# Kernel optimization log

Measured on AMD Instinct MI355X. Metric: run time of the kernel, lower is better.

## Reference

```python
import jax, jax.numpy as jnp
from jax import lax
import numpy as np

N = 4096      # nnodes
D = 64        # embed_dim
R = 128       # nodes per region
G = N // R    # 32 regions (contiguous blocks)
BIG = 1e9     # 'no edge' cost (scipy MST treats zero-similarity entries as absent edges)


def setup_inputs() -> dict:
    key = jax.random.key(0)
    emb = jax.random.normal(key, (N, D), dtype=jnp.float32) * 0.05  # nn.Embedding weight (xavier-like scale)
    region_id = jnp.arange(N) // R
    inter_mask = (region_id[:, None] != region_id[None, :]).astype(jnp.float32)  # block off-diagonal buffer
    return {"emb_weight": emb, "inter_mask": inter_mask, "inter_budget": 1024}


def _prim_forest_mask(W):
    """Prim's algorithm on dense cost matrix W [R,R] (BIG = missing edge).
    Returns symmetric 0/1 minimum-spanning-FOREST edge mask, matching
    scipy.sparse.csgraph.minimum_spanning_tree on the same graph (weights distinct)."""
    r = W.shape[0]

    def step(carry, _):
        in_tree, key_, parent, mask = carry
        km = jnp.where(in_tree, BIG, key_)
        u = jnp.argmin(km)                          # cheapest node to attach
        valid = (km[u] < BIG * 0.5).astype(W.dtype)  # BIG key => start new component, no edge
        p = parent[u]
        mask = mask.at[u, p].add(valid)
        mask = mask.at[p, u].add(valid)
        in_tree = in_tree.at[u].set(True)
        wu = W[u]
        improve = (~in_tree) & (wu < key_)
        key_ = jnp.where(improve, wu, key_)
        parent = jnp.where(improve, u, parent)
        return (in_tree, key_, parent, mask), None

    in_tree0 = jnp.zeros(r, dtype=bool).at[0].set(True)
    key0 = W[0]
    parent0 = jnp.zeros(r, dtype=jnp.int32)
    mask0 = jnp.zeros_like(W)
    (_, _, _, mask), _ = lax.scan(step, (in_tree0, key0, parent0, mask0), None, length=r - 1)
    return (mask > 0).astype(W.dtype)


def reference(emb_weight, inter_mask, inter_budget):
    # adj_dense = relu(tanh(E E^T))  [N,N]
    adj = jax.nn.relu(jnp.tanh(emb_weight @ emb_weight.T))
    adj_ng = lax.stop_gradient(adj)  # torch: MST input is .detach(); top-k indices carry no grad

    # ---- intra: per-region MST (max spanning forest of similarity == min SF of -sim) ----
    blocks = adj_ng.reshape(G, R, G, R)[jnp.arange(G), :, jnp.arange(G), :]  # [G,R,R] diagonal blocks
    eye = jnp.eye(R, dtype=bool)
    W = jnp.where((blocks > 0) & ~eye, -blocks, BIG)  # zero similarity => no edge (scipy semantics)
    intra_blocks = jax.vmap(_prim_forest_mask)(W)     # [G,R,R]
    idx = jnp.arange(N).reshape(G, R)
    intra = jnp.zeros((N, N), adj.dtype).at[idx[:, :, None], idx[:, None, :]].set(intra_blocks)
    intra = intra * (1.0 - jnp.eye(N, dtype=adj.dtype))  # fill_diagonal_(0)

    # ---- inter: global top-k over upper-triangular masked similarities ----
    flat = jnp.triu(adj_ng * inter_mask, k=1).reshape(-1)  # [N*N]
    k = int(inter_budget)  # == min(budget, nnz(inter_mask)//2); budget is smaller by construction
    _, top_idx = lax.top_k(flat, k)
    inter_sel = jnp.zeros(N * N, adj.dtype).at[top_idx].set(1.0).reshape(N, N)
    inter_sel = inter_sel + inter_sel.T

    final_mask = ((intra + inter_sel) > 0).astype(adj.dtype)
    return adj * final_mask
```

## Files before the change

### kernel.cpp

```cpp
#include <hip/hip_runtime.h>

#define NN 4096
#define DD 64
#define RR 128
#define GG 32
constexpr unsigned BIGH = 0xCE6E6B28u;
constexpr unsigned FLOOR_KEY = 0x3D000000u;
constexpr int FLOORB = 0x3D0;
constexpr int NBINS  = 64;

constexpr int WS_FH   = 0;
constexpr int WS_ECNT = 2051;
constexpr int WS_CCNT = 2052;
constexpr int WS_MIJ  = 2112;
constexpr int WS_MV   = WS_MIJ + 4096;
constexpr int WS_EI   = WS_MV + 4096;
constexpr int WS_EJ   = WS_EI + 8192;
constexpr int WS_EV   = WS_EJ + 8192;
constexpr int WS_CK   = WS_EV + 8192;
constexpr int WS_CI   = WS_CK + 8192;
constexpr int EDGE_CAP = 8192;
constexpr int CAND_CAP = 8192;

__global__ void init_kernel(unsigned* ws) {
  for (int b = threadIdx.x; b < 2112; b += 1024) ws[b] = 0;
}

__device__ __forceinline__ void pair_decode(int p, int& gi, int& gj) {
  gi = 0;
  int rem = p;
  while (rem >= GG - 1 - gi) { rem -= GG - 1 - gi; ++gi; }
  gj = gi + 1 + rem;
}

__device__ __forceinline__ void scan_bins(const unsigned* __restrict__ ws, unsigned k,
                                          unsigned* shm ,
                                          unsigned& tlo, unsigned& thi, unsigned& rem) {
  const int t = threadIdx.x;
  if (t < NBINS) shm[t] = ws[WS_FH + FLOORB + t];
  __syncthreads();
  if (t == 0) {
    unsigned cum = 0;
    int fb = FLOORB;
    unsigned r = 0;
    for (int b = NBINS - 1; b >= 0; --b) {
      unsigned c = shm[b];
      if (cum + c >= k) { fb = FLOORB + b; r = k - cum; break; }
      cum += c;
    }
    shm[64] = ((unsigned)fb) << 20;
    shm[65] = ((unsigned)(fb + 1)) << 20;
    shm[66] = r;
  }
  __syncthreads();
  tlo = shm[64];
  thi = shm[65];
  rem = shm[66];
}

__global__ __launch_bounds__(256) void gemm_adj_kernel(const float* __restrict__ E,
                                                       float* __restrict__ adj,
                                                       unsigned* __restrict__ ws) {
  const int ti = blockIdx.y, tj = blockIdx.x;
  const bool rdiag = (ti >> 1) == (tj >> 1);
  if (tj < ti && !rdiag) return;
  const bool cross = (tj >> 1) > (ti >> 1);

  __shared__ float4 As4[64 * 16];
  __shared__ float4 Bs4[64 * 16];
  __shared__ unsigned h[NBINS];
  const float4* E4 = (const float4*)E;
  const int bi = ti * 64, bj = tj * 64;
  const int tid = threadIdx.x;

  if (tid < NBINS) h[tid] = 0;

#pragma unroll
  for (int it = 0; it < 4; ++it) {
    int row = (tid >> 4) + it * 16;
    int g = tid & 15;
    int sw = g ^ ((row >> 2) & 7);
    As4[row * 16 + sw] = E4[(bi + row) * 16 + g];
    Bs4[row * 16 + sw] = E4[(bj + row) * 16 + g];
  }
  __syncthreads();

  const int i0 = (tid >> 4) * 4;
  const int j0 = (tid & 15) * 4;
  const int sa = (i0 >> 2) & 7;
  const int sb = (j0 >> 2) & 7;
  float acc[4][4] = {};
#pragma unroll 2
  for (int k4 = 0; k4 < 16; ++k4) {
    float4 av[4], bv[4];
#pragma unroll
    for (int r = 0; r < 4; ++r) av[r] = As4[(i0 + r) * 16 + (k4 ^ sa)];
#pragma unroll
    for (int c = 0; c < 4; ++c) bv[c] = Bs4[(j0 + c) * 16 + (k4 ^ sb)];
#pragma unroll
    for (int r = 0; r < 4; ++r)
#pragma unroll
      for (int c = 0; c < 4; ++c) {
        acc[r][c] += av[r].x * bv[c].x;
        acc[r][c] += av[r].y * bv[c].y;
        acc[r][c] += av[r].z * bv[c].z;
        acc[r][c] += av[r].w * bv[c].w;
      }
  }
#pragma unroll
  for (int r = 0; r < 4; ++r) {
    float4 o;
    float* p = &o.x;
#pragma unroll
    for (int c = 0; c < 4; ++c) {
      float t = tanhf(acc[r][c]);
      p[c] = t > 0.f ? t : 0.f;
    }
    *(float4*)(adj + (size_t)(bi + i0 + r) * NN + bj + j0) = o;
    if (cross) {
#pragma unroll
      for (int c = 0; c < 4; ++c) {
        unsigned key = __float_as_uint(p[c]);
        if (key >= FLOOR_KEY) atomicAdd(&h[(key >> 20) - FLOORB], 1u);
      }
    }
  }
  if (cross) {
    __syncthreads();
    if (tid < NBINS) {
      unsigned c = h[tid];
      if (c) atomicAdd(&ws[WS_FH + FLOORB + tid], c);
    }
  }
}

template <int CTRL>
__device__ __forceinline__ unsigned dpp_umin(unsigned v) {
  unsigned o = (unsigned)__builtin_amdgcn_update_dpp((int)v, (int)v, CTRL, 0xF, 0xF, false);
  return o < v ? o : v;
}
__device__ __forceinline__ unsigned xfneg(float a) {
  return ~__float_as_uint(a) & 0x7FFFFFFFu;
}

__global__ __launch_bounds__(64) void mst_kernel(const float* __restrict__ adj, unsigned* ws) {
  __shared__ float W[RR * RR];
  const int g = blockIdx.x, l = threadIdx.x, base = g * RR;
  float4* W4 = (float4*)W;
  const float4* A4 = (const float4*)adj;

#pragma unroll
  for (int n = 0; n < 64; ++n) {
    int f = l + 64 * n;
    W4[f] = A4[(size_t)(base + (f >> 5)) * (NN / 4) + (base >> 2) + (f & 31)];
  }
  __syncthreads();

  const int n0 = l, n1 = l + 64;
  float a0 = W[n0], a1 = W[n1];
  unsigned key0 = (n0 != 0 && a0 > 0.f) ? xfneg(a0) : BIGH;
  unsigned key1 = (a1 > 0.f) ? xfneg(a1) : BIGH;
  bool in0 = (l == 0), in1 = false;
  int par0 = 0, par1 = 0;
  unsigned e0ij = 0xFFFFFFFFu, e1ij = 0xFFFFFFFFu;
  float e0v = 0.f, e1v = 0.f;

  for (int it = 0; it < RR - 1; ++it) {
    const unsigned kA = in0 ? BIGH : key0;
    const unsigned kB = in1 ? BIGH : key1;
    unsigned km = kA < kB ? kA : kB;
    km = dpp_umin<0xB1>(km);
    km = dpp_umin<0x4E>(km);
    km = dpp_umin<0x141>(km);
    km = dpp_umin<0x140>(km);
    const unsigned r0 = (unsigned)__builtin_amdgcn_readlane((int)km, 15);
    const unsigned r1 = (unsigned)__builtin_amdgcn_readlane((int)km, 31);
    const unsigned r2 = (unsigned)__builtin_amdgcn_readlane((int)km, 47);
    const unsigned r3 = (unsigned)__builtin_amdgcn_readlane((int)km, 63);
    const unsigned ma = r0 < r1 ? r0 : r1;
    const unsigned mb = r2 < r3 ? r2 : r3;
    const unsigned m = ma < mb ? ma : mb;

    const unsigned long long b0 = __ballot(kA == m);
    const unsigned long long b1 = __ballot(kB == m);
    const int u = b0 ? (__ffsll((unsigned long long)b0) - 1)
                     : (64 + __ffsll((unsigned long long)b1) - 1);

    const int p0 = __builtin_amdgcn_readlane(par0, u & 63);
    const int p1 = __builtin_amdgcn_readlane(par1, u & 63);
    const int par = (u >> 6) ? p1 : p0;
    unsigned pij = 0xFFFFFFFFu;
    float pv = 0.f;
    if ((int)m >= 0) {
      pij = ((unsigned)(base + u) << 12) | (unsigned)(base + par);
      pv = __uint_as_float(~m & 0x7FFFFFFFu);
    }
    const bool mine = (l == (it & 63));
    if (it & 64) { if (mine) { e1ij = pij; e1v = pv; } }
    else         { if (mine) { e0ij = pij; e0v = pv; } }

    in0 = in0 || (u == n0);
    in1 = in1 || (u == n1);
    float w0v = W[u * RR + n0];
    float w1v = W[u * RR + n1];
    unsigned w0 = (w0v > 0.f && n0 != u) ? xfneg(w0v) : BIGH;
    unsigned w1 = (w1v > 0.f && n1 != u) ? xfneg(w1v) : BIGH;
    if (!in0 && w0 < key0) { key0 = w0; par0 = u; }
    if (!in1 && w1 < key1) { key1 = w1; par1 = u; }
  }
  ws[WS_MIJ + base + l] = e0ij;
  ws[WS_MIJ + base + 64 + l] = e1ij;
  ((float*)(ws + WS_MV))[base + l] = e0v;
  ((float*)(ws + WS_MV))[base + 64 + l] = e1v;
}

__global__ __launch_bounds__(256) void collect_kernel(const float* __restrict__ adj,
                                                      unsigned* ws, const int* budget) {
  __shared__ unsigned shm[67];
  unsigned tlo, thi, rem;
  scan_bins(ws, (unsigned)budget[0], shm, tlo, thi, rem);
  (void)rem;
  int gi, gj;
  pair_decode(blockIdx.x, gi, gj);
  const float4* a4 = (const float4*)adj;
  for (int e = threadIdx.x; e < RR * 32; e += 256) {
    int r = e >> 5, c4 = e & 31;
    float4 v = a4[(size_t)(gi * RR + r) * (NN / 4) + gj * 32 + c4];
    float comp[4] = {v.x, v.y, v.z, v.w};
#pragma unroll
    for (int c = 0; c < 4; ++c) {
      float x = comp[c];
      if (!(x > 0.f)) continue;
      unsigned key = __float_as_uint(x);
      if (key < tlo) continue;
      int i = gi * RR + r, j = gj * RR + c4 * 4 + c;
      if (key >= thi) {
        unsigned slot = atomicAdd(ws + WS_ECNT, 1u);
        if (slot < EDGE_CAP) {
          ((int*)(ws + WS_EI))[slot] = i;
          ((int*)(ws + WS_EJ))[slot] = j;
          ((float*)(ws + WS_EV))[slot] = x;
        }
      } else {
        unsigned s2 = atomicAdd(ws + WS_CCNT, 1u);
        if (s2 < CAND_CAP) {
          ws[WS_CK + s2] = key;
          ws[WS_CI + s2] = (unsigned)((i << 12) | j);
        }
      }
    }
  }
}

__global__ __launch_bounds__(1024) void topk_kernel(unsigned* ws, const int* budget) {
  __shared__ unsigned long long s[CAND_CAP];
  __shared__ unsigned shm[67];
  unsigned tlo, thi, rem;
  scan_bins(ws, (unsigned)budget[0], shm, tlo, thi, rem);
  (void)tlo; (void)thi;
  const int t = threadIdx.x;
  unsigned n = ws[WS_CCNT];
  if (n > CAND_CAP) n = CAND_CAP;
  unsigned m = 2;
  while (m < n) m <<= 1;
  for (int i = t; i < (int)m; i += 1024) {
    unsigned long long v = 0ull;
    if (i < (int)n)
      v = ((unsigned long long)ws[WS_CK + i] << 32) |
          (unsigned long long)(0x00FFFFFFu - ws[WS_CI + i]);
    s[i] = v;
  }
  for (unsigned size = 2; size <= m; size <<= 1)
    for (unsigned stride = size >> 1; stride; stride >>= 1) {
      __syncthreads();
      for (unsigned i = t; i < m / 2; i += 1024) {
        unsigned lo = ((i & ~(stride - 1)) << 1) | (i & (stride - 1));
        unsigned hi = lo | stride;
        bool up = ((lo & size) == 0);
        unsigned long long a = s[lo], b = s[hi];
        if ((a > b) == up) { s[lo] = b; s[hi] = a; }
      }
    }
  __syncthreads();
  for (unsigned p = t; p < rem; p += 1024) {
    unsigned long long v = s[m - 1 - p];
    if (v == 0ull) continue;
    unsigned key = (unsigned)(v >> 32);
    unsigned idx = 0x00FFFFFFu - (unsigned)(v & 0xFFFFFFFFull);
    unsigned slot = atomicAdd(ws + WS_ECNT, 1u);
    if (slot < EDGE_CAP) {
      ((int*)(ws + WS_EI))[slot] = (int)(idx >> 12);
      ((int*)(ws + WS_EJ))[slot] = (int)(idx & 4095u);
      ((float*)(ws + WS_EV))[slot] = __uint_as_float(key);
    }
  }
}

__global__ __launch_bounds__(256) void zero_scatter_kernel(const unsigned* __restrict__ ws,
                                                           float* __restrict__ out) {
  const int bid = blockIdx.x;
  const int r0 = bid * 16;
  float4* out4 = (float4*)(out + (size_t)r0 * NN);
  const float4 z = make_float4(0.f, 0.f, 0.f, 0.f);
  for (int e = threadIdx.x; e < 16 * (NN / 4); e += 256) out4[e] = z;
  __syncthreads();
  unsigned cnt = ws[WS_ECNT];
  if (cnt > EDGE_CAP) cnt = EDGE_CAP;
  const int tot = 4096 + (int)cnt;
  for (int e = threadIdx.x; e < tot; e += 256) {
    int i, j;
    float v;
    if (e < 4096) {
      unsigned pij = ws[WS_MIJ + e];
      if (pij == 0xFFFFFFFFu) continue;
      i = (int)(pij >> 12);
      j = (int)(pij & 4095u);
      v = ((const float*)(ws + WS_MV))[e];
    } else {
      int q = e - 4096;
      i = ((const int*)(ws + WS_EI))[q];
      j = ((const int*)(ws + WS_EJ))[q];
      v = ((const float*)(ws + WS_EV))[q];
    }
    if ((i >> 4) == bid) out[(size_t)i * NN + j] = v;
    if ((j >> 4) == bid) out[(size_t)j * NN + i] = v;
  }
}

extern "C" void kernel_launch(void* const* d_in, const int* in_sizes, int n_in,
                              void* d_out, int out_size, void* d_ws, size_t ws_size,
                              hipStream_t stream) {
  const float* E      = (const float*)d_in[0];
  const int*   budget = (const int*)d_in[2];
  float*    adj = (float*)d_out;
  unsigned* ws  = (unsigned*)d_ws;

  init_kernel<<<1, 1024, 0, stream>>>(ws);
  gemm_adj_kernel<<<dim3(NN / 64, NN / 64), 256, 0, stream>>>(E, adj, ws);
  mst_kernel<<<GG, 64, 0, stream>>>(adj, ws);
  collect_kernel<<<GG * (GG - 1) / 2, 256, 0, stream>>>(adj, ws, budget);
  topk_kernel<<<1, 1024, 0, stream>>>(ws, budget);
  zero_scatter_kernel<<<256, 256, 0, stream>>>(ws, adj);
}
```

Baseline: 254.6 us.

## Fuse MST, candidate collection and top-k into one kernel with last-block completion

Merges the per-region MST, inter-region candidate collection and bitonic top-k into a single launch. The first 32 blocks run Prim's MST while the remaining blocks collect candidates concurrently, and the last collect block to finish (detected with an atomic done counter) performs the sort. This removes two kernel launches and lets MST overlap with collection. In exchange the sort runs with 256 threads instead of 1024, and every block reserves a large shared buffer, which may limit occupancy.

```diff
diff --git a/kernel.cpp b/kernel.cpp
--- a/kernel.cpp
+++ b/kernel.cpp
@@ -8,10 +8,12 @@
 constexpr unsigned FLOOR_KEY = 0x3D000000u;
 constexpr int FLOORB = 0x3D0;
 constexpr int NBINS  = 64;
+constexpr int NPAIRS = GG * (GG - 1) / 2;
 
 constexpr int WS_FH   = 0;
 constexpr int WS_ECNT = 2051;
 constexpr int WS_CCNT = 2052;
+constexpr int WS_DONE = 2054;
 constexpr int WS_MIJ  = 2112;
 constexpr int WS_MV   = WS_MIJ + 4096;
 constexpr int WS_EI   = WS_MV + 4096;
@@ -143,87 +145,91 @@
   return ~__float_as_uint(a) & 0x7FFFFFFFu;
 }
 
-__global__ __launch_bounds__(64) void mst_kernel(const float* __restrict__ adj, unsigned* ws) {
-  __shared__ float W[RR * RR];
-  const int g = blockIdx.x, l = threadIdx.x, base = g * RR;
-  float4* W4 = (float4*)W;
-  const float4* A4 = (const float4*)adj;
-
-#pragma unroll
-  for (int n = 0; n < 64; ++n) {
-    int f = l + 64 * n;
-    W4[f] = A4[(size_t)(base + (f >> 5)) * (NN / 4) + (base >> 2) + (f & 31)];
-  }
-  __syncthreads();
-
-  const int n0 = l, n1 = l + 64;
-  float a0 = W[n0], a1 = W[n1];
-  unsigned key0 = (n0 != 0 && a0 > 0.f) ? xfneg(a0) : BIGH;
-  unsigned key1 = (a1 > 0.f) ? xfneg(a1) : BIGH;
-  bool in0 = (l == 0), in1 = false;
-  int par0 = 0, par1 = 0;
-  unsigned e0ij = 0xFFFFFFFFu, e1ij = 0xFFFFFFFFu;
-  float e0v = 0.f, e1v = 0.f;
-
-  for (int it = 0; it < RR - 1; ++it) {
-    const unsigned kA = in0 ? BIGH : key0;
-    const unsigned kB = in1 ? BIGH : key1;
-    unsigned km = kA < kB ? kA : kB;
-    km = dpp_umin<0xB1>(km);
-    km = dpp_umin<0x4E>(km);
-    km = dpp_umin<0x141>(km);
-    km = dpp_umin<0x140>(km);
-    const unsigned r0 = (unsigned)__builtin_amdgcn_readlane((int)km, 15);
-    const unsigned r1 = (unsigned)__builtin_amdgcn_readlane((int)km, 31);
-    const unsigned r2 = (unsigned)__builtin_amdgcn_readlane((int)km, 47);
-    const unsigned r3 = (unsigned)__builtin_amdgcn_readlane((int)km, 63);
-    const unsigned ma = r0 < r1 ? r0 : r1;
-    const unsigned mb = r2 < r3 ? r2 : r3;
-    const unsigned m = ma < mb ? ma : mb;
-
-    const unsigned long long b0 = __ballot(kA == m);
-    const unsigned long long b1 = __ballot(kB == m);
-    const int u = b0 ? (__ffsll((unsigned long long)b0) - 1)
-                     : (64 + __ffsll((unsigned long long)b1) - 1);
-
-    const int p0 = __builtin_amdgcn_readlane(par0, u & 63);
-    const int p1 = __builtin_amdgcn_readlane(par1, u & 63);
-    const int par = (u >> 6) ? p1 : p0;
-    unsigned pij = 0xFFFFFFFFu;
-    float pv = 0.f;
-    if ((int)m >= 0) {
-      pij = ((unsigned)(base + u) << 12) | (unsigned)(base + par);
-      pv = __uint_as_float(~m & 0x7FFFFFFFu);
-    }
-    const bool mine = (l == (it & 63));
-    if (it & 64) { if (mine) { e1ij = pij; e1v = pv; } }
-    else         { if (mine) { e0ij = pij; e0v = pv; } }
-
-    in0 = in0 || (u == n0);
-    in1 = in1 || (u == n1);
-    float w0v = W[u * RR + n0];
-    float w1v = W[u * RR + n1];
-    unsigned w0 = (w0v > 0.f && n0 != u) ? xfneg(w0v) : BIGH;
-    unsigned w1 = (w1v > 0.f && n1 != u) ? xfneg(w1v) : BIGH;
-    if (!in0 && w0 < key0) { key0 = w0; par0 = u; }
-    if (!in1 && w1 < key1) { key1 = w1; par1 = u; }
-  }
-  ws[WS_MIJ + base + l] = e0ij;
-  ws[WS_MIJ + base + 64 + l] = e1ij;
-  ((float*)(ws + WS_MV))[base + l] = e0v;
-  ((float*)(ws + WS_MV))[base + 64 + l] = e1v;
-}
-
-__global__ __launch_bounds__(256) void collect_kernel(const float* __restrict__ adj,
-                                                      unsigned* ws, const int* budget) {
-  __shared__ unsigned shm[67];
+__global__ __launch_bounds__(256) void mega_kernel(const float* __restrict__ adj,
+                                                   unsigned* ws, const int* budget) {
+  __shared__ unsigned long long buf64[8192];
+  __shared__ unsigned shm[68];
+  const int tid = threadIdx.x;
+
+  if (blockIdx.x < GG) {
+    float* W = (float*)buf64;
+    const int g = blockIdx.x, base = g * RR;
+    float4* W4 = (float4*)W;
+    const float4* A4 = (const float4*)adj;
+#pragma unroll
+    for (int n = 0; n < 16; ++n) {
+      int f = tid + 256 * n;
+      W4[f] = A4[(size_t)(base + (f >> 5)) * (NN / 4) + (base >> 2) + (f & 31)];
+    }
+    __syncthreads();
+    if (tid < 64) {
+      const int l = tid;
+      const int n0 = l, n1 = l + 64;
+      float a0 = W[n0], a1 = W[n1];
+      unsigned key0 = (n0 != 0 && a0 > 0.f) ? xfneg(a0) : BIGH;
+      unsigned key1 = (a1 > 0.f) ? xfneg(a1) : BIGH;
+      bool in0 = (l == 0), in1 = false;
+      int par0 = 0, par1 = 0;
+      unsigned e0ij = 0xFFFFFFFFu, e1ij = 0xFFFFFFFFu;
+      float e0v = 0.f, e1v = 0.f;
+
+      for (int it = 0; it < RR - 1; ++it) {
+        const unsigned kA = in0 ? BIGH : key0;
+        const unsigned kB = in1 ? BIGH : key1;
+        unsigned km = kA < kB ? kA : kB;
+        km = dpp_umin<0xB1>(km);
+        km = dpp_umin<0x4E>(km);
+        km = dpp_umin<0x141>(km);
+        km = dpp_umin<0x140>(km);
+        const unsigned r0 = (unsigned)__builtin_amdgcn_readlane((int)km, 15);
+        const unsigned r1 = (unsigned)__builtin_amdgcn_readlane((int)km, 31);
+        const unsigned r2 = (unsigned)__builtin_amdgcn_readlane((int)km, 47);
+        const unsigned r3 = (unsigned)__builtin_amdgcn_readlane((int)km, 63);
+        const unsigned ma = r0 < r1 ? r0 : r1;
+        const unsigned mb = r2 < r3 ? r2 : r3;
+        const unsigned m = ma < mb ? ma : mb;
+
+        const unsigned long long b0 = __ballot(kA == m);
+        const unsigned long long b1 = __ballot(kB == m);
+        const int u = b0 ? (__ffsll((unsigned long long)b0) - 1)
+                         : (64 + __ffsll((unsigned long long)b1) - 1);
+
+        const int p0 = __builtin_amdgcn_readlane(par0, u & 63);
+        const int p1 = __builtin_amdgcn_readlane(par1, u & 63);
+        const int par = (u >> 6) ? p1 : p0;
+        unsigned pij = 0xFFFFFFFFu;
+        float pv = 0.f;
+        if ((int)m >= 0) {
+          pij = ((unsigned)(base + u) << 12) | (unsigned)(base + par);
+          pv = __uint_as_float(~m & 0x7FFFFFFFu);
+        }
+        const bool mine = (l == (it & 63));
+        if (it & 64) { if (mine) { e1ij = pij; e1v = pv; } }
+        else         { if (mine) { e0ij = pij; e0v = pv; } }
+
+        in0 = in0 || (u == n0);
+        in1 = in1 || (u == n1);
+        float w0v = W[u * RR + n0];
+        float w1v = W[u * RR + n1];
+        unsigned w0 = (w0v > 0.f && n0 != u) ? xfneg(w0v) : BIGH;
+        unsigned w1 = (w1v > 0.f && n1 != u) ? xfneg(w1v) : BIGH;
+        if (!in0 && w0 < key0) { key0 = w0; par0 = u; }
+        if (!in1 && w1 < key1) { key1 = w1; par1 = u; }
+      }
+      ws[WS_MIJ + base + l] = e0ij;
+      ws[WS_MIJ + base + 64 + l] = e1ij;
+      ((float*)(ws + WS_MV))[base + l] = e0v;
+      ((float*)(ws + WS_MV))[base + 64 + l] = e1v;
+    }
+    return;
+  }
+
   unsigned tlo, thi, rem;
   scan_bins(ws, (unsigned)budget[0], shm, tlo, thi, rem);
-  (void)rem;
   int gi, gj;
-  pair_decode(blockIdx.x, gi, gj);
+  pair_decode((int)blockIdx.x - GG, gi, gj);
   const float4* a4 = (const float4*)adj;
-  for (int e = threadIdx.x; e < RR * 32; e += 256) {
+  for (int e = tid; e < RR * 32; e += 256) {
     int r = e >> 5, c4 = e & 31;
     float4 v = a4[(size_t)(gi * RR + r) * (NN / 4) + gj * 32 + c4];
     float comp[4] = {v.x, v.y, v.z, v.w};
@@ -250,40 +256,42 @@
       }
     }
   }
-}
-
-__global__ __launch_bounds__(1024) void topk_kernel(unsigned* ws, const int* budget) {
-  __shared__ unsigned long long s[CAND_CAP];
-  __shared__ unsigned shm[67];
-  unsigned tlo, thi, rem;
-  scan_bins(ws, (unsigned)budget[0], shm, tlo, thi, rem);
-  (void)tlo; (void)thi;
-  const int t = threadIdx.x;
+
+  __threadfence();
+  __syncthreads();
+  if (tid == 0) {
+    unsigned old = atomicAdd(ws + WS_DONE, 1u);
+    shm[67] = (old == (unsigned)(NPAIRS - 1)) ? 1u : 0u;
+  }
+  __syncthreads();
+  if (!shm[67]) return;
+  __threadfence();
+
   unsigned n = ws[WS_CCNT];
   if (n > CAND_CAP) n = CAND_CAP;
-  unsigned m = 2;
-  while (m < n) m <<= 1;
-  for (int i = t; i < (int)m; i += 1024) {
+  unsigned m2 = 2;
+  while (m2 < n) m2 <<= 1;
+  for (int i = tid; i < (int)m2; i += 256) {
     unsigned long long v = 0ull;
     if (i < (int)n)
       v = ((unsigned long long)ws[WS_CK + i] << 32) |
           (unsigned long long)(0x00FFFFFFu - ws[WS_CI + i]);
-    s[i] = v;
-  }
-  for (unsigned size = 2; size <= m; size <<= 1)
+    buf64[i] = v;
+  }
+  for (unsigned size = 2; size <= m2; size <<= 1)
     for (unsigned stride = size >> 1; stride; stride >>= 1) {
       __syncthreads();
-      for (unsigned i = t; i < m / 2; i += 1024) {
+      for (unsigned i = tid; i < m2 / 2; i += 256) {
         unsigned lo = ((i & ~(stride - 1)) << 1) | (i & (stride - 1));
         unsigned hi = lo | stride;
         bool up = ((lo & size) == 0);
-        unsigned long long a = s[lo], b = s[hi];
-        if ((a > b) == up) { s[lo] = b; s[hi] = a; }
-      }
-    }
-  __syncthreads();
-  for (unsigned p = t; p < rem; p += 1024) {
-    unsigned long long v = s[m - 1 - p];
+        unsigned long long a = buf64[lo], b = buf64[hi];
+        if ((a > b) == up) { buf64[lo] = b; buf64[hi] = a; }
+      }
+    }
+  __syncthreads();
+  for (unsigned p = tid; p < rem; p += 256) {
+    unsigned long long v = buf64[m2 - 1 - p];
     if (v == 0ull) continue;
     unsigned key = (unsigned)(v >> 32);
     unsigned idx = 0x00FFFFFFu - (unsigned)(v & 0xFFFFFFFFull);
@@ -337,8 +345,6 @@
 
   init_kernel<<<1, 1024, 0, stream>>>(ws);
   gemm_adj_kernel<<<dim3(NN / 64, NN / 64), 256, 0, stream>>>(E, adj, ws);
-  mst_kernel<<<GG, 64, 0, stream>>>(adj, ws);
-  collect_kernel<<<GG * (GG - 1) / 2, 256, 0, stream>>>(adj, ws, budget);
-  topk_kernel<<<1, 1024, 0, stream>>>(ws, budget);
+  mega_kernel<<<GG + NPAIRS, 256, 0, stream>>>(adj, ws, budget);
   zero_scatter_kernel<<<256, 256, 0, stream>>>(ws, adj);
 }
```

After: 266.9 us. +4.8%, slower.
